# Optimization experiments

Hardware: AMD Instinct MI355X
Metric: run time of the kernel (lower is better)

## Reference

```python
import jax, jax.numpy as jnp
import numpy as np

K, D = 4096, 256
BETA, DECAY, EPS = 0.25, 0.99, 1e-05
B = 32768


def setup_inputs() -> dict:
    key = jax.random.key(0)
    k1, k2, k3, k4 = jax.random.split(key, 4)
    return {
        "z_e": jax.random.normal(k1, (B, D), dtype=jnp.float32),
        "codebook": jax.random.normal(k2, (K, D), dtype=jnp.float32),
        "ema_cluster_size": jax.random.uniform(k3, (K,), dtype=jnp.float32),
        "ema_weight": jax.random.normal(k4, (K, D), dtype=jnp.float32),
    }


def reference(z_e, codebook, ema_cluster_size, ema_weight):
    z_e = z_e.astype(jnp.float32)
    # squared L2 distances: ||z||^2 - 2 z.C^T + ||C||^2  (chunking in torch is
    # purely a memory optimization; math is identical)
    e_norm = jnp.sum(z_e * z_e, axis=1, keepdims=True)            # [B,1]
    c_norm = jnp.sum(codebook * codebook, axis=1)                  # [K]
    dists = e_norm - 2.0 * (z_e @ codebook.T) + c_norm[None, :]    # [B,K]
    idx = jnp.argmin(dists, axis=1)                                # [B] int

    z_q = codebook[idx]                                            # [B,d] gather

    # EMA codebook update (no_grad in torch)
    counts = jnp.zeros((K,), jnp.float32).at[idx].add(1.0)         # bincount
    new_cluster = ema_cluster_size * DECAY + counts * (1.0 - DECAY)
    dw = jnp.zeros((K, D), jnp.float32).at[idx].add(z_e)           # index_add_
    new_ema_weight = ema_weight * DECAY + dw * (1.0 - DECAY)
    n = jnp.sum(new_cluster)
    cluster_size = (new_cluster + EPS) / (n + K * EPS) * n
    new_codebook = new_ema_weight / cluster_size[:, None]

    z_q_ste = z_e + jax.lax.stop_gradient(z_q - z_e)
    commit = BETA * jnp.mean((z_e - z_q) ** 2)
    return (z_q_ste, idx, commit, new_codebook, new_cluster, new_ema_weight)
```

## Files before the change

kernel.cpp:

```cpp
#include <hip/hip_runtime.h>

#define KC 4096
#define DD 256
#define BB 32768
#define P_BETA 0.25f
#define P_DECAY 0.99f
#define P_EPS 1e-5f
#define TAU 0.5f
#define CHUNK 32

typedef __attribute__((ext_vector_type(8))) short bf16x8;
typedef __attribute__((ext_vector_type(4))) float f32x4;

static __device__ __forceinline__ unsigned short f2bf(float f) {
    unsigned int u = __float_as_uint(f);
    unsigned int r = (u + 0x7fffu + ((u >> 16) & 1u)) >> 16;
    return (unsigned short)r;
}
static __device__ __forceinline__ void gload_lds16(const void* g, void* s) {
    __builtin_amdgcn_global_load_lds(
        (const __attribute__((address_space(1))) unsigned int*)g,
        (__attribute__((address_space(3))) unsigned int*)s, 16, 0, 0);
}

#define ZBLK (BB * DD / 4 / 256)
#define CBLK (KC * DD / 4 / 256)
__global__ __launch_bounds__(256) void convert_all_kernel(
    const float* __restrict__ z, const float* __restrict__ cb,
    unsigned short* __restrict__ zb, unsigned short* __restrict__ cbb,
    float* __restrict__ cn, int* __restrict__ cnt) {
    const int b = blockIdx.x;
    if (b < ZBLK) {
        int t = b * 256 + threadIdx.x;
        float4 v = ((const float4*)z)[t];
        *(ushort4*)&zb[(size_t)t * 4] =
            make_ushort4(f2bf(v.x), f2bf(v.y), f2bf(v.z), f2bf(v.w));
    } else if (b < ZBLK + CBLK) {
        int t = (b - ZBLK) * 256 + threadIdx.x;
        int lane = threadIdx.x & 63;
        int row = (b - ZBLK) * 4 + (threadIdx.x >> 6);
        float4 v = ((const float4*)cb)[t];
        *(ushort4*)&cbb[(size_t)t * 4] =
            make_ushort4(f2bf(v.x), f2bf(v.y), f2bf(v.z), f2bf(v.w));
        float s = v.x * v.x + v.y * v.y + v.z * v.z + v.w * v.w;
#pragma unroll
        for (int m = 32; m; m >>= 1) s += __shfl_xor(s, m);
        if (lane == 0) cn[row] = s;
    } else {
        int4* p = (int4*)cnt;
        int4 zv = make_int4(0, 0, 0, 0);
#pragma unroll
        for (int j = 0; j < 4; ++j) p[threadIdx.x * 4 + j] = zv;
    }
}

__global__ __launch_bounds__(256, 2) void
mfma_argmin_kernel(const unsigned short* __restrict__ zb,
                   const unsigned short* __restrict__ cbb,
                   const float* __restrict__ cn,
                   float4* __restrict__ cand) {
    __shared__ unsigned short As[128 * 128];
    __shared__ unsigned short Bs[2][128 * 64];

    const int tid = threadIdx.x;
    const int l = tid & 63, w = tid >> 6;
    const int xcd = blockIdx.x & 7;
    const int half = xcd >> 2;
    const int rb = (blockIdx.x >> 3) * 4 + (xcd & 3);
    const int row0 = rb * 128;
    const int col0 = half * 2048;
    const int wm = w & 1, wn = w >> 1;
    const int m_off = wm * 64, n_off = wn * 64;
    const int lm = l & 15, lq = l >> 4;

    {
        const int lr = (l >> 4);
        const int c = l & 15;
#pragma unroll
        for (int i = 0; i < 8; ++i) {
            const int r = i * 16 + w * 4 + lr;
            gload_lds16(zb + (size_t)(row0 + r) * DD + ((c ^ (r & 7)) * 8),
                        &As[(i * 16 + w * 4) * 128]);
        }
    }

    const int srow = l >> 3;
    const int scol = ((l & 7) ^ srow) * 8;
    const int g0 = w * 4;
    auto stageB = [&](int buf, int s) {
        const int kcn = (s >> 2) * 128;
        const int dcn = (s & 3) * 64;
#pragma unroll
        for (int j = 0; j < 4; ++j) {
            const int g = g0 + j;
            const int br = col0 + kcn + g * 8 + srow;
            gload_lds16(cbb + (size_t)br * DD + dcn + scol, &Bs[buf][g * 512]);
        }
    };
    stageB(0, 0);

    bf16x8 afr[4][4];
#pragma unroll
    for (int tm = 0; tm < 4; ++tm) {
        const size_t grow = (size_t)(row0 + m_off + tm * 16 + lm) * DD;
#pragma unroll
        for (int t = 0; t < 4; ++t)
            afr[tm][t] = *(const bf16x8*)&zb[grow + 128 + t * 32 + lq * 8];
    }

    __syncthreads();

    float best[16];
    int bidx[16];
#pragma unroll
    for (int s = 0; s < 16; ++s) { best[s] = 3.4e38f; bidx[s] = 0; }

    int cur = 0;
    for (int kc = 0; kc < 2048; kc += 128) {
        f32x4 acc[4][4];
#pragma unroll
        for (int a = 0; a < 4; ++a)
#pragma unroll
            for (int b = 0; b < 4; ++b) acc[a][b] = (f32x4){0.f, 0.f, 0.f, 0.f};

#pragma unroll
        for (int dc = 0; dc < 4; ++dc) {
            const int ns = (kc >> 7) * 4 + dc + 1;
            if (ns < 64) stageB(cur ^ 1, ns);
#pragma unroll
            for (int ks = 0; ks < 2; ++ks) {
                bf16x8 af[4], bfr[4];
#pragma unroll
                for (int tn = 0; tn < 4; ++tn) {
                    int r = n_off + tn * 16 + lm;
                    bfr[tn] = *(const bf16x8*)&Bs[cur][r * 64 + (((ks * 4 + lq) ^ (r & 7)) * 8)];
                }
                if (dc < 2) {
                    const int cbi = dc * 8 + ks * 4 + lq;
#pragma unroll
                    for (int tm = 0; tm < 4; ++tm) {
                        int r = m_off + tm * 16 + lm;
                        af[tm] = *(const bf16x8*)&As[r * 128 + ((cbi ^ (r & 7)) * 8)];
                    }
                } else {
#pragma unroll
                    for (int tm = 0; tm < 4; ++tm) af[tm] = afr[tm][(dc - 2) * 2 + ks];
                }
#pragma unroll
                for (int tm = 0; tm < 4; ++tm)
#pragma unroll
                    for (int tn = 0; tn < 4; ++tn)
                        acc[tm][tn] = __builtin_amdgcn_mfma_f32_16x16x32_bf16(
                            af[tm], bfr[tn], acc[tm][tn], 0, 0, 0);
            }
            __syncthreads();
            cur ^= 1;
        }

#pragma unroll
        for (int tn = 0; tn < 4; ++tn) {
            const int col = col0 + kc + n_off + tn * 16 + lm;
            const float cnv = cn[col];
#pragma unroll
            for (int tm = 0; tm < 4; ++tm)
#pragma unroll
                for (int r = 0; r < 4; ++r) {
                    float dist = fmaf(-2.0f, acc[tm][tn][r], cnv);
                    int s = tm * 4 + r;
                    if (dist < best[s]) { best[s] = dist; bidx[s] = col; }
                }
        }
    }

    float v2[16];
    int i2[16];
#pragma unroll
    for (int s = 0; s < 16; ++s) { v2[s] = 3.4e38f; i2[s] = 0x7fffffff; }
#pragma unroll
    for (int m = 1; m < 16; m <<= 1) {
#pragma unroll
        for (int s = 0; s < 16; ++s) {
            float w1 = __shfl_xor(best[s], m); int j1 = __shfl_xor(bidx[s], m);
            float w2 = __shfl_xor(v2[s], m);   int j2 = __shfl_xor(i2[s], m);
            bool b = (w1 < best[s]) || (w1 == best[s] && j1 < bidx[s]);
            if (b) {
                bool c = (best[s] < w2) || (best[s] == w2 && bidx[s] < j2);
                v2[s] = c ? best[s] : w2; i2[s] = c ? bidx[s] : j2;
                best[s] = w1; bidx[s] = j1;
            } else {
                bool c = (w1 < v2[s]) || (w1 == v2[s] && j1 < i2[s]);
                v2[s] = c ? w1 : v2[s]; i2[s] = c ? j1 : i2[s];
            }
        }
    }

    float4* red = (float4*)As;
    if (lm == 0) {
#pragma unroll
        for (int tm = 0; tm < 4; ++tm)
#pragma unroll
            for (int r = 0; r < 4; ++r) {
                int s = tm * 4 + r;
                int row_local = m_off + tm * 16 + lq * 4 + r;
                red[wn * 128 + row_local] =
                    make_float4(best[s], __int_as_float(bidx[s]), v2[s], __int_as_float(i2[s]));
            }
    }
    __syncthreads();
    if (tid < 128) {
        float4 a = red[tid], b = red[128 + tid];
        float av1 = a.x, av2 = a.z; int ai1 = __float_as_int(a.y), ai2 = __float_as_int(a.w);
        float bv1 = b.x, bv2 = b.z; int bi1 = __float_as_int(b.y), bi2 = __float_as_int(b.w);
        float v1o, v2o; int i1o, i2o;
        bool bb = (bv1 < av1) || (bv1 == av1 && bi1 < ai1);
        if (bb) {
            v1o = bv1; i1o = bi1;
            bool c = (av1 < bv2) || (av1 == bv2 && ai1 < bi2);
            v2o = c ? av1 : bv2; i2o = c ? ai1 : bi2;
        } else {
            v1o = av1; i1o = ai1;
            bool c = (bv1 < av2) || (bv1 == av2 && bi1 < ai2);
            v2o = c ? bv1 : av2; i2o = c ? bi1 : ai2;
        }
        cand[(size_t)half * BB + row0 + tid] =
            make_float4(v1o, __int_as_float(i1o), v2o, __int_as_float(i2o));
    }
}

__global__ __launch_bounds__(256) void merge_refine_kernel(
    const float4* __restrict__ cand, const float* __restrict__ z,
    const float* __restrict__ cb, const float* __restrict__ cn,
    int* __restrict__ idx_i, float* __restrict__ idx_f,
    int* __restrict__ cnt, float* __restrict__ dw) {
    int i = blockIdx.x * 256 + threadIdx.x;
    {
        float4 zv4 = make_float4(0.f, 0.f, 0.f, 0.f);
        float4* dp = (float4*)dw;
        int base = i * 8;
#pragma unroll
        for (int j = 0; j < 8; ++j) dp[base + j] = zv4;
    }
    float4 a = cand[i], b = cand[(size_t)BB + i];
    float av1 = a.x, av2 = a.z; int ai1 = __float_as_int(a.y), ai2 = __float_as_int(a.w);
    float bv1 = b.x, bv2 = b.z; int bi1 = __float_as_int(b.y), bi2 = __float_as_int(b.w);
    float v1o, v2o; int i1o, i2o;
    bool bb = (bv1 < av1) || (bv1 == av1 && bi1 < ai1);
    if (bb) {
        v1o = bv1; i1o = bi1;
        bool c = (av1 < bv2) || (av1 == bv2 && ai1 < bi2);
        v2o = c ? av1 : bv2; i2o = c ? ai1 : bi2;
    } else {
        v1o = av1; i1o = ai1;
        bool c = (bv1 < av2) || (bv1 == av2 && bi1 < ai2);
        v2o = c ? bv1 : av2; i2o = c ? bi1 : ai2;
    }
    int kb = i1o;
    if (v2o - v1o < TAU) {
        const float4* zr = (const float4*)(z + (size_t)i * DD);
        const float4* c1 = (const float4*)(cb + (size_t)i1o * DD);
        const float4* c2 = (const float4*)(cb + (size_t)i2o * DD);
        float s1x = 0, s1y = 0, s1z = 0, s1w = 0;
        float s2x = 0, s2y = 0, s2z = 0, s2w = 0;
        for (int j = 0; j < 64; ++j) {
            float4 zv = zr[j], p = c1[j], q = c2[j];
            s1x = fmaf(zv.x, p.x, s1x); s1y = fmaf(zv.y, p.y, s1y);
            s1z = fmaf(zv.z, p.z, s1z); s1w = fmaf(zv.w, p.w, s1w);
            s2x = fmaf(zv.x, q.x, s2x); s2y = fmaf(zv.y, q.y, s2y);
            s2z = fmaf(zv.z, q.z, s2z); s2w = fmaf(zv.w, q.w, s2w);
        }
        float d1 = cn[i1o] - 2.f * ((s1x + s1y) + (s1z + s1w));
        float d2 = cn[i2o] - 2.f * ((s2x + s2y) + (s2z + s2w));
        if (d2 < d1 || (d2 == d1 && i2o < i1o)) kb = i2o;
    }
    idx_i[i] = kb;
    idx_f[i] = (float)kb;
    atomicAdd(&cnt[kb], 1);
}

__global__ __launch_bounds__(256) void prefix_kernel(const int* __restrict__ cnt,
                                                     int* __restrict__ cursor) {
    __shared__ int ls[257];
    const int t = threadIdx.x;
    int local[16];
    int s = 0;
#pragma unroll
    for (int j = 0; j < 16; ++j) { local[j] = s; s += cnt[t * 16 + j]; }
    ls[t + 1] = s;
    __syncthreads();
    if (t == 0) {
        ls[0] = 0;
        for (int j = 1; j <= 256; ++j) ls[j] += ls[j - 1];
    }
    __syncthreads();
    int off = ls[t];
#pragma unroll
    for (int j = 0; j < 16; ++j) cursor[t * 16 + j] = off + local[j];
}

__global__ __launch_bounds__(256) void zq_commit_scatter_kernel(
    const float* __restrict__ z, const float* __restrict__ cb,
    const int* __restrict__ idx_i, float* __restrict__ zq,
    float* __restrict__ commit_parts, int* __restrict__ cursor,
    int* __restrict__ row_of) {
    const int w = threadIdx.x >> 6, l = threadIdx.x & 63;
    const int i = blockIdx.x * 4 + w;
    const int k = idx_i[i];
    float4 zv = ((const float4*)z)[(size_t)i * 64 + l];
    float4 cv = ((const float4*)cb)[(size_t)k * 64 + l];
    ((float4*)zq)[(size_t)i * 64 + l] = cv;
    float dx = zv.x - cv.x, dy = zv.y - cv.y, dz = zv.z - cv.z, dq = zv.w - cv.w;
    float s = dx * dx + dy * dy + dz * dz + dq * dq;
#pragma unroll
    for (int m = 32; m; m >>= 1) s += __shfl_xor(s, m);
    __shared__ float ls[4];
    if (l == 0) {
        ls[w] = s;
        int pos = atomicAdd(&cursor[k], 1);
        row_of[pos] = i | (k << 16);
    }
    __syncthreads();
    if (threadIdx.x == 0) commit_parts[blockIdx.x] = ls[0] + ls[1] + ls[2] + ls[3];
}

__global__ __launch_bounds__(256) void bucket_cluster_kernel(
    const float* __restrict__ z, const int* __restrict__ row_of,
    float* __restrict__ dw, const float* __restrict__ ema_cs,
    const int* __restrict__ cnt, const float* __restrict__ commit_parts,
    float* __restrict__ out_cluster, float* __restrict__ n_ws,
    float* __restrict__ out_commit) {
    const int t = threadIdx.x;
    if (blockIdx.x == BB / CHUNK) {
        float cs = 0.f;
        for (int j = t; j < BB / 4; j += 256) cs += commit_parts[j];
        float ns = 0.f;
        for (int j = t; j < KC; j += 256) {
            float nc = ema_cs[j] * P_DECAY + (float)cnt[j] * (1.0f - P_DECAY);
            out_cluster[j] = nc;
            ns += nc;
        }
#pragma unroll
        for (int m = 32; m; m >>= 1) { cs += __shfl_xor(cs, m); ns += __shfl_xor(ns, m); }
        __shared__ float lc[4], ln[4];
        if ((t & 63) == 0) { lc[t >> 6] = cs; ln[t >> 6] = ns; }
        __syncthreads();
        if (t == 0) {
            *out_commit = P_BETA * (lc[0] + lc[1] + lc[2] + lc[3]) / (float)((size_t)BB * DD);
            *n_ws = ln[0] + ln[1] + ln[2] + ln[3];
        }
        return;
    }
    __shared__ int pk[CHUNK];
    const int p0 = blockIdx.x * CHUNK;
    if (t < CHUNK) pk[t] = row_of[p0 + t];
    __syncthreads();
    float acc = 0.f;
    int kprev = pk[0] >> 16;
#pragma unroll 4
    for (int j = 0; j < CHUNK; ++j) {
        int p = pk[j];
        int r = p & 0xffff, k = p >> 16;
        if (k != kprev) {
            atomicAdd(&dw[(size_t)kprev * DD + t], acc);
            acc = 0.f;
            kprev = k;
        }
        acc += z[(size_t)r * DD + t];
    }
    atomicAdd(&dw[(size_t)kprev * DD + t], acc);
}

__global__ __launch_bounds__(256) void finalize_kernel(const float* __restrict__ ema_w,
                                                       const float* __restrict__ dw,
                                                       const float* __restrict__ out_cluster,
                                                       const float* __restrict__ n_ws,
                                                       float* __restrict__ out_ema_w,
                                                       float* __restrict__ out_codebook) {
    const size_t id = (size_t)blockIdx.x * 256 + threadIdx.x;
    const int k = (int)(id >> 8);
    const float n = *n_ws;
    float nw = ema_w[id] * P_DECAY + dw[id] * (1.0f - P_DECAY);
    out_ema_w[id] = nw;
    float cl = out_cluster[k];
    float csz = (cl + P_EPS) / (n + (float)KC * P_EPS) * n;
    out_codebook[id] = nw / csz;
}

extern "C" void kernel_launch(void* const* d_in, const int* in_sizes, int n_in,
                              void* d_out, int out_size, void* d_ws, size_t ws_size,
                              hipStream_t stream) {
    const float* z      = (const float*)d_in[0];
    const float* cb     = (const float*)d_in[1];
    const float* ema_cs = (const float*)d_in[2];
    const float* ema_w  = (const float*)d_in[3];

    float4* cand = (float4*)d_ws;
    unsigned short* zb = (unsigned short*)(cand + 2 * (size_t)BB);
    unsigned short* cbb = zb + (size_t)BB * DD;
    float* dw = (float*)(cbb + (size_t)KC * DD);
    float* c_norm = dw + (size_t)KC * DD;
    int* idx_i = (int*)(c_norm + KC);
    int* cnt = idx_i + BB;
    int* cursor = cnt + KC;
    int* row_of = cursor + KC;
    float* commit_parts = (float*)(row_of + BB);
    float* n_ws = commit_parts + BB / 4;

    float* out        = (float*)d_out;
    float* o_zq       = out;
    float* o_idx      = o_zq + (size_t)BB * DD;
    float* o_commit   = o_idx + BB;
    float* o_codebook = o_commit + 1;
    float* o_cluster  = o_codebook + (size_t)KC * DD;
    float* o_emaw     = o_cluster + KC;

    convert_all_kernel<<<ZBLK + CBLK + 1, 256, 0, stream>>>(z, cb, zb, cbb, c_norm, cnt);
    mfma_argmin_kernel<<<(BB / 128) * 2, 256, 0, stream>>>(zb, cbb, c_norm, cand);
    merge_refine_kernel<<<BB / 256, 256, 0, stream>>>(cand, z, cb, c_norm, idx_i,
                                                      o_idx, cnt, dw);
    prefix_kernel<<<1, 256, 0, stream>>>(cnt, cursor);
    zq_commit_scatter_kernel<<<BB / 4, 256, 0, stream>>>(z, cb, idx_i, o_zq,
                                                         commit_parts, cursor, row_of);
    bucket_cluster_kernel<<<BB / CHUNK + 1, 256, 0, stream>>>(z, row_of, dw, ema_cs,
                                                              cnt, commit_parts,
                                                              o_cluster, n_ws, o_commit);
    finalize_kernel<<<(KC * DD) / 256, 256, 0, stream>>>(ema_w, dw, o_cluster, n_ws,
                                                         o_emaw, o_codebook);
    (void)in_sizes; (void)n_in; (void)out_size; (void)ws_size;
}
```

Before: 255.6 us.

## Fuse prefix and finalize kernels via last-block and grid-wide atomic barriers

Result: slower. 408.3 us (+59.8%).

```diff
diff --git a/kernel.cpp b/kernel.cpp
--- a/kernel.cpp
+++ b/kernel.cpp
@@ -28,7 +28,7 @@
 __global__ __launch_bounds__(256) void convert_all_kernel(
     const float* __restrict__ z, const float* __restrict__ cb,
     unsigned short* __restrict__ zb, unsigned short* __restrict__ cbb,
-    float* __restrict__ cn, int* __restrict__ cnt) {
+    float* __restrict__ cn, int* __restrict__ cnt, int* __restrict__ done) {
     const int b = blockIdx.x;
     if (b < ZBLK) {
         int t = b * 256 + threadIdx.x;
@@ -51,10 +51,12 @@
         int4 zv = make_int4(0, 0, 0, 0);
 #pragma unroll
         for (int j = 0; j < 4; ++j) p[threadIdx.x * 4 + j] = zv;
-    }
-}
-
-__global__ __launch_bounds__(256, 2) void
+        if (threadIdx.x < 4) done[threadIdx.x] = 0;
+    }
+}
+
+__global__ __launch_bounds__(256)
+__attribute__((amdgpu_waves_per_eu(2, 2))) void
 mfma_argmin_kernel(const unsigned short* __restrict__ zb,
                    const unsigned short* __restrict__ cbb,
                    const float* __restrict__ cn,
@@ -231,7 +233,8 @@
     const float4* __restrict__ cand, const float* __restrict__ z,
     const float* __restrict__ cb, const float* __restrict__ cn,
     int* __restrict__ idx_i, float* __restrict__ idx_f,
-    int* __restrict__ cnt, float* __restrict__ dw) {
+    int* __restrict__ cnt, float* __restrict__ dw,
+    int* __restrict__ cursor, int* __restrict__ done) {
     int i = blockIdx.x * 256 + threadIdx.x;
     {
         float4 zv4 = make_float4(0.f, 0.f, 0.f, 0.f);
@@ -275,26 +278,37 @@
     idx_i[i] = kb;
     idx_f[i] = (float)kb;
     atomicAdd(&cnt[kb], 1);
-}
-
-__global__ __launch_bounds__(256) void prefix_kernel(const int* __restrict__ cnt,
-                                                     int* __restrict__ cursor) {
-    __shared__ int ls[257];
-    const int t = threadIdx.x;
-    int local[16];
-    int s = 0;
-#pragma unroll
-    for (int j = 0; j < 16; ++j) { local[j] = s; s += cnt[t * 16 + j]; }
-    ls[t + 1] = s;
-    __syncthreads();
-    if (t == 0) {
-        ls[0] = 0;
-        for (int j = 1; j <= 256; ++j) ls[j] += ls[j - 1];
-    }
-    __syncthreads();
-    int off = ls[t];
-#pragma unroll
-    for (int j = 0; j < 16; ++j) cursor[t * 16 + j] = off + local[j];
+
+    __shared__ int lastflag;
+    __syncthreads();
+    if (threadIdx.x == 0) {
+        int r = __hip_atomic_fetch_add(&done[0], 1, __ATOMIC_ACQ_REL,
+                                       __HIP_MEMORY_SCOPE_AGENT);
+        lastflag = (r == (int)gridDim.x - 1);
+    }
+    __syncthreads();
+    if (lastflag) {
+        __shared__ int ls[257];
+        const int t = threadIdx.x;
+        int local[16];
+        int s = 0;
+#pragma unroll
+        for (int j = 0; j < 16; ++j) {
+            local[j] = s;
+            s += __hip_atomic_load(&cnt[t * 16 + j], __ATOMIC_RELAXED,
+                                   __HIP_MEMORY_SCOPE_AGENT);
+        }
+        ls[t + 1] = s;
+        __syncthreads();
+        if (t == 0) {
+            ls[0] = 0;
+            for (int j = 1; j <= 256; ++j) ls[j] += ls[j - 1];
+        }
+        __syncthreads();
+        int off = ls[t];
+#pragma unroll
+        for (int j = 0; j < 16; ++j) cursor[t * 16 + j] = off + local[j];
+    }
 }
 
 __global__ __launch_bounds__(256) void zq_commit_scatter_kernel(
@@ -327,7 +341,9 @@
     float* __restrict__ dw, const float* __restrict__ ema_cs,
     const int* __restrict__ cnt, const float* __restrict__ commit_parts,
     float* __restrict__ out_cluster, float* __restrict__ n_ws,
-    float* __restrict__ out_commit) {
+    float* __restrict__ out_commit, const float* __restrict__ ema_w,
+    float* __restrict__ out_ema_w, float* __restrict__ out_codebook,
+    int* __restrict__ done) {
     const int t = threadIdx.x;
     if (blockIdx.x == BB / CHUNK) {
         float cs = 0.f;
@@ -347,42 +363,50 @@
             *out_commit = P_BETA * (lc[0] + lc[1] + lc[2] + lc[3]) / (float)((size_t)BB * DD);
             *n_ws = ln[0] + ln[1] + ln[2] + ln[3];
         }
-        return;
-    }
-    __shared__ int pk[CHUNK];
-    const int p0 = blockIdx.x * CHUNK;
-    if (t < CHUNK) pk[t] = row_of[p0 + t];
-    __syncthreads();
-    float acc = 0.f;
-    int kprev = pk[0] >> 16;
+    } else {
+        __shared__ int pk[CHUNK];
+        const int p0 = blockIdx.x * CHUNK;
+        if (t < CHUNK) pk[t] = row_of[p0 + t];
+        __syncthreads();
+        float acc = 0.f;
+        int kprev = pk[0] >> 16;
 #pragma unroll 4
-    for (int j = 0; j < CHUNK; ++j) {
-        int p = pk[j];
-        int r = p & 0xffff, k = p >> 16;
-        if (k != kprev) {
-            atomicAdd(&dw[(size_t)kprev * DD + t], acc);
-            acc = 0.f;
-            kprev = k;
-        }
-        acc += z[(size_t)r * DD + t];
-    }
-    atomicAdd(&dw[(size_t)kprev * DD + t], acc);
-}
-
-__global__ __launch_bounds__(256) void finalize_kernel(const float* __restrict__ ema_w,
-                                                       const float* __restrict__ dw,
-                                                       const float* __restrict__ out_cluster,
-                                                       const float* __restrict__ n_ws,
-                                                       float* __restrict__ out_ema_w,
-                                                       float* __restrict__ out_codebook) {
-    const size_t id = (size_t)blockIdx.x * 256 + threadIdx.x;
-    const int k = (int)(id >> 8);
+        for (int j = 0; j < CHUNK; ++j) {
+            int p = pk[j];
+            int r = p & 0xffff, k = p >> 16;
+            if (k != kprev) {
+                atomicAdd(&dw[(size_t)kprev * DD + t], acc);
+                acc = 0.f;
+                kprev = k;
+            }
+            acc += z[(size_t)r * DD + t];
+        }
+        atomicAdd(&dw[(size_t)kprev * DD + t], acc);
+    }
+
+    __syncthreads();
+    if (t == 0) {
+        __hip_atomic_fetch_add(&done[1], 1, __ATOMIC_RELEASE,
+                               __HIP_MEMORY_SCOPE_AGENT);
+        int v;
+        do {
+            v = __hip_atomic_load(&done[1], __ATOMIC_ACQUIRE,
+                                  __HIP_MEMORY_SCOPE_AGENT);
+            if (v < (int)gridDim.x) __builtin_amdgcn_s_sleep(8);
+        } while (v < (int)gridDim.x);
+    }
+    __syncthreads();
+
     const float n = *n_ws;
-    float nw = ema_w[id] * P_DECAY + dw[id] * (1.0f - P_DECAY);
-    out_ema_w[id] = nw;
-    float cl = out_cluster[k];
-    float csz = (cl + P_EPS) / (n + (float)KC * P_EPS) * n;
-    out_codebook[id] = nw / csz;
+    const size_t stride = (size_t)gridDim.x * 256;
+    for (size_t id = (size_t)blockIdx.x * 256 + t; id < (size_t)KC * DD; id += stride) {
+        const int k = (int)(id >> 8);
+        float nw = ema_w[id] * P_DECAY + dw[id] * (1.0f - P_DECAY);
+        out_ema_w[id] = nw;
+        float cl = out_cluster[k];
+        float csz = (cl + P_EPS) / (n + (float)KC * P_EPS) * n;
+        out_codebook[id] = nw / csz;
+    }
 }
 
 extern "C" void kernel_launch(void* const* d_in, const int* in_sizes, int n_in,
@@ -404,6 +428,7 @@
     int* row_of = cursor + KC;
     float* commit_parts = (float*)(row_of + BB);
     float* n_ws = commit_parts + BB / 4;
+    int* done = (int*)(n_ws + 1);
 
     float* out        = (float*)d_out;
     float* o_zq       = out;
@@ -413,17 +438,15 @@
     float* o_cluster  = o_codebook + (size_t)KC * DD;
     float* o_emaw     = o_cluster + KC;
 
-    convert_all_kernel<<<ZBLK + CBLK + 1, 256, 0, stream>>>(z, cb, zb, cbb, c_norm, cnt);
+    convert_all_kernel<<<ZBLK + CBLK + 1, 256, 0, stream>>>(z, cb, zb, cbb, c_norm,
+                                                            cnt, done);
     mfma_argmin_kernel<<<(BB / 128) * 2, 256, 0, stream>>>(zb, cbb, c_norm, cand);
     merge_refine_kernel<<<BB / 256, 256, 0, stream>>>(cand, z, cb, c_norm, idx_i,
-                                                      o_idx, cnt, dw);
-    prefix_kernel<<<1, 256, 0, stream>>>(cnt, cursor);
+                                                      o_idx, cnt, dw, cursor, done);
     zq_commit_scatter_kernel<<<BB / 4, 256, 0, stream>>>(z, cb, idx_i, o_zq,
                                                          commit_parts, cursor, row_of);
-    bucket_cluster_kernel<<<BB / CHUNK + 1, 256, 0, stream>>>(z, row_of, dw, ema_cs,
-                                                              cnt, commit_parts,
-                                                              o_cluster, n_ws, o_commit);
-    finalize_kernel<<<(KC * DD) / 256, 256, 0, stream>>>(ema_w, dw, o_cluster, n_ws,
-                                                         o_emaw, o_codebook);
+    bucket_cluster_kernel<<<BB / CHUNK + 1, 256, 0, stream>>>(
+        z, row_of, dw, ema_cs, cnt, commit_parts, o_cluster, n_ws, o_commit,
+        ema_w, o_emaw, o_codebook, done);
     (void)in_sizes; (void)n_in; (void)out_size; (void)ws_size;
 }
```
